# Performance work log

Hardware: AMD Instinct MI355X
Metric: run time of the kernel (lower is better)

The kernel has to match this reference:

```python
import jax, jax.numpy as jnp
import numpy as np

ITERS = 3

def squash(s, axis):
    # v = (|s|^2 / (1 + |s|^2)) * s / |s|
    sn = jnp.sum(s * s, axis=axis, keepdims=True)
    return sn / (1.0 + sn) * s / jnp.sqrt(sn)

def setup_inputs() -> dict:
    key = jax.random.key(0)
    k1, k2 = jax.random.split(key)
    b, B, C, P2, f = 8, 144, 16, 16, 12
    u = jax.random.normal(k1, (b, B, C, P2, f, f), dtype=jnp.float32)
    a = jax.random.uniform(k2, (b, B, f, f), dtype=jnp.float32)
    return {"u": u, "a": a}

def reference(u, a):
    # u: (b, B, C, P2, f, f); a: (b, B, f, f)
    b, B, C, P2, f, _ = u.shape
    # r: (b, B, C, 1, f, f), initialized uniform over C scaled by activation
    r = jnp.broadcast_to(a[:, :, None, None, :, :] * (1.0 / C), (b, B, C, 1, f, f))
    v = None
    for i in range(ITERS):
        c = jax.nn.softmax(r, axis=2)                       # over C
        v = squash(jnp.sum(c * u, axis=1, keepdims=True), axis=3)  # (b,1,C,P2,f,f)
        if i != ITERS - 1:
            r = r + jnp.sum(u * v, axis=3, keepdims=True)   # agreement over psize
    a_out = jnp.sqrt(jnp.sum(v * v, axis=3, keepdims=True))  # (b,1,C,1,f,f)
    return (jnp.squeeze(v, axis=1), jnp.squeeze(a_out, axis=(1, 3)))
```

## Files before the change

kernel.cpp:

```cpp
#include <hip/hip_runtime.h>
#include <math.h>


#define NB 8
#define BDIM 144
#define CDIM 16
#define PDIM 16
#define SDIM 144
#define PT 16
#define BC 16
#define NPT (SDIM / PT)
#define NBC (BDIM / BC)
#define VELEMS (NB * CDIM * PDIM * SDIM)
#define AELEMS (NB * CDIM * SDIM)

__global__ __launch_bounds__(256) void s_kernel(const float* __restrict__ u,
                                                const float* __restrict__ a,
                                                const float* __restrict__ V,
                                                float* __restrict__ s,
                                                int iter) {
  __shared__ float Vt[CDIM][PDIM][PT];
  __shared__ float lbuf[2][CDIM][PT + 1];

  const int tid = threadIdx.x;
  const int pos = tid & 15;
  const int c = tid >> 4;
  const int b = blockIdx.z;
  const int posg = blockIdx.y * PT + pos;
  const int B0 = blockIdx.x * BC;

  if (iter > 0) {
    const int vb = ((b * CDIM + c) * PDIM) * SDIM + posg;
#pragma unroll
    for (int p = 0; p < PDIM; ++p) Vt[c][p][pos] = V[vb + p * SDIM];
  }
  __syncthreads();

  float sacc[PDIM];
#pragma unroll
  for (int p = 0; p < PDIM; ++p) sacc[p] = 0.f;

  for (int Bi = B0; Bi < B0 + BC; ++Bi) {
    float uv[PDIM];
    const float* ub = u + ((size_t)((b * BDIM + Bi) * CDIM + c) * PDIM) * SDIM + posg;
#pragma unroll
    for (int p = 0; p < PDIM; ++p) uv[p] = ub[p * SDIM];

    float w;
    if (iter == 0) {
      w = 1.0f / CDIM;
    } else {
      float dot = 0.f;
#pragma unroll
      for (int p = 0; p < PDIM; ++p) dot += uv[p] * Vt[c][p][pos];
      const float logit = a[(b * BDIM + Bi) * SDIM + posg] * (1.0f / CDIM) + dot;
      const int pb = Bi & 1;
      lbuf[pb][c][pos] = logit;
      __syncthreads();
      float m = -1e30f;
#pragma unroll
      for (int c2 = 0; c2 < CDIM; ++c2) m = fmaxf(m, lbuf[pb][c2][pos]);
      float sum = 0.f;
#pragma unroll
      for (int c2 = 0; c2 < CDIM; ++c2) sum += __expf(lbuf[pb][c2][pos] - m);
      w = __expf(logit - m) / sum;
    }
#pragma unroll
    for (int p = 0; p < PDIM; ++p) sacc[p] += w * uv[p];
  }

  const int sb = ((b * CDIM + c) * PDIM) * SDIM + posg;
#pragma unroll
  for (int p = 0; p < PDIM; ++p) atomicAdd(&s[sb + p * SDIM], sacc[p]);
}

__global__ __launch_bounds__(256) void q_kernel(float* __restrict__ s,
                                                float* __restrict__ V,
                                                float* __restrict__ out_v,
                                                float* __restrict__ out_a,
                                                int iter) {
  const int gid = blockIdx.x * 256 + threadIdx.x;
  const int b = gid / (CDIM * SDIM);
  const int rem = gid - b * (CDIM * SDIM);
  const int c = rem / SDIM;
  const int posg = rem - c * SDIM;
  const int base = ((b * CDIM + c) * PDIM) * SDIM + posg;

  float sv[PDIM];
  float sn = 0.f;
#pragma unroll
  for (int p = 0; p < PDIM; ++p) {
    const float x = s[base + p * SDIM];
    sv[p] = x;
    sn += x * x;
  }
  const float scale = sn / (1.0f + sn) * rsqrtf(sn);

  if (iter < 2) {
#pragma unroll
    for (int p = 0; p < PDIM; ++p) {
      V[base + p * SDIM] += sv[p] * scale;
      s[base + p * SDIM] = 0.f;
    }
  } else {
    float vv = 0.f;
#pragma unroll
    for (int p = 0; p < PDIM; ++p) {
      const float v = sv[p] * scale;
      out_v[base + p * SDIM] = v;
      vv += v * v;
    }
    out_a[gid] = sqrtf(vv);
  }
}

extern "C" void kernel_launch(void* const* d_in, const int* in_sizes, int n_in,
                              void* d_out, int out_size, void* d_ws, size_t ws_size,
                              hipStream_t stream) {
  const float* u = (const float*)d_in[0];
  const float* a = (const float*)d_in[1];
  float* V = (float*)d_ws;
  float* s = V + VELEMS;
  float* out_v = (float*)d_out;
  float* out_a = out_v + VELEMS;

  hipMemsetAsync(d_ws, 0, (size_t)2 * VELEMS * sizeof(float), stream);

  const dim3 gS(NBC, NPT, NB);
  for (int it = 0; it < 3; ++it) {
    s_kernel<<<gS, 256, 0, stream>>>(u, a, V, s, it);
    q_kernel<<<AELEMS / 256, 256, 0, stream>>>(s, V, out_v, out_a, it);
  }
}
```

Before: 356.6 us.

## Prefetch u loads, specialize first iteration, drop softmax max pass, halve B chunk

Restructures the routing kernel. A dedicated path for the first iteration does a plain sum without the softmax. Later iterations double-buffer the u register loads, stage the activation tile in shared memory, and skip the max-subtraction pass in the softmax, using a fast reciprocal. The B chunk per block is halved to raise the number of blocks in flight. This trades more atomics and the loss of the max-stabilized softmax, which could overflow for large logits, for better latency hiding and less per-step work.

```diff
diff --git a/kernel.cpp b/kernel.cpp
--- a/kernel.cpp
+++ b/kernel.cpp
@@ -8,9 +8,10 @@
 #define PDIM 16
 #define SDIM 144
 #define PT 16
-#define BC 16
+#define BC 8
 #define NPT (SDIM / PT)
 #define NBC (BDIM / BC)
+#define USTRIDE (CDIM * PDIM * SDIM)
 #define VELEMS (NB * CDIM * PDIM * SDIM)
 #define AELEMS (NB * CDIM * SDIM)
 
@@ -20,7 +21,8 @@
                                                 float* __restrict__ s,
                                                 int iter) {
   __shared__ float Vt[CDIM][PDIM][PT];
-  __shared__ float lbuf[2][CDIM][PT + 1];
+  __shared__ float ebuf[2][CDIM][PT + 1];
+  __shared__ float atile[BC][PT];
 
   const int tid = threadIdx.x;
   const int pos = tid & 15;
@@ -29,42 +31,62 @@
   const int posg = blockIdx.y * PT + pos;
   const int B0 = blockIdx.x * BC;
 
-  if (iter > 0) {
-    const int vb = ((b * CDIM + c) * PDIM) * SDIM + posg;
-#pragma unroll
-    for (int p = 0; p < PDIM; ++p) Vt[c][p][pos] = V[vb + p * SDIM];
-  }
-  __syncthreads();
+  const float* ubase =
+      u + ((size_t)((b * BDIM + B0) * CDIM + c) * PDIM) * SDIM + posg;
 
   float sacc[PDIM];
 #pragma unroll
   for (int p = 0; p < PDIM; ++p) sacc[p] = 0.f;
 
-  for (int Bi = B0; Bi < B0 + BC; ++Bi) {
-    float uv[PDIM];
-    const float* ub = u + ((size_t)((b * BDIM + Bi) * CDIM + c) * PDIM) * SDIM + posg;
+  if (iter == 0) {
+#pragma unroll 2
+    for (int j = 0; j < BC; ++j) {
+      const float* ub = ubase + (size_t)j * USTRIDE;
 #pragma unroll
-    for (int p = 0; p < PDIM; ++p) uv[p] = ub[p * SDIM];
+      for (int p = 0; p < PDIM; ++p) sacc[p] += ub[p * SDIM];
+    }
+    const int sb = ((b * CDIM + c) * PDIM) * SDIM + posg;
+#pragma unroll
+    for (int p = 0; p < PDIM; ++p)
+      atomicAdd(&s[sb + p * SDIM], sacc[p] * (1.0f / CDIM));
+    return;
+  }
 
-    float w;
-    if (iter == 0) {
-      w = 1.0f / CDIM;
-    } else {
-      float dot = 0.f;
+  {
+    const int vb = ((b * CDIM + c) * PDIM) * SDIM + posg;
 #pragma unroll
-      for (int p = 0; p < PDIM; ++p) dot += uv[p] * Vt[c][p][pos];
-      const float logit = a[(b * BDIM + Bi) * SDIM + posg] * (1.0f / CDIM) + dot;
-      const int pb = Bi & 1;
-      lbuf[pb][c][pos] = logit;
-      __syncthreads();
-      float m = -1e30f;
+    for (int p = 0; p < PDIM; ++p) Vt[c][p][pos] = V[vb + p * SDIM];
+    if (tid < BC * PT) {
+      const int j = tid >> 4;
+      atile[j][pos] =
+          a[(b * BDIM + B0 + j) * SDIM + blockIdx.y * PT + pos] * (1.0f / CDIM);
+    }
+  }
+  __syncthreads();
+
+  float uvbuf[2][PDIM];
 #pragma unroll
-      for (int c2 = 0; c2 < CDIM; ++c2) m = fmaxf(m, lbuf[pb][c2][pos]);
-      float sum = 0.f;
+  for (int p = 0; p < PDIM; ++p) uvbuf[0][p] = ubase[p * SDIM];
+
 #pragma unroll
-      for (int c2 = 0; c2 < CDIM; ++c2) sum += __expf(lbuf[pb][c2][pos] - m);
-      w = __expf(logit - m) / sum;
+  for (int j = 0; j < BC; ++j) {
+    float* uv = uvbuf[j & 1];
+    float* uvn = uvbuf[(j + 1) & 1];
+    if (j + 1 < BC) {
+      const float* ub = ubase + (size_t)(j + 1) * USTRIDE;
+#pragma unroll
+      for (int p = 0; p < PDIM; ++p) uvn[p] = ub[p * SDIM];
     }
+    float dot = 0.f;
+#pragma unroll
+    for (int p = 0; p < PDIM; ++p) dot += uv[p] * Vt[c][p][pos];
+    const float e = __expf(atile[j][pos] + dot);
+    ebuf[j & 1][c][pos] = e;
+    __syncthreads();
+    float sum = 0.f;
+#pragma unroll
+    for (int c2 = 0; c2 < CDIM; ++c2) sum += ebuf[j & 1][c2][pos];
+    const float w = e * __builtin_amdgcn_rcpf(sum);
 #pragma unroll
     for (int p = 0; p < PDIM; ++p) sacc[p] += w * uv[p];
   }
```

Measured after the change: 355.3 us. No clear change (-0.4%).

## Transpose u to position-major layout once, use vectorized loads and shuffle softmax

Applied to the files above, without the earlier changes.

The first pass reads u, writes a transposed copy with psize innermost to workspace, and accumulates the uniform-weight s in the same sweep. Later passes read that copy with float4 loads and do the softmax over C with wave shuffles instead of LDS and barriers. The max subtraction is dropped, and the final activation is taken directly from the squash factor. This adds one full extra write of u (about 100MB) and relies on the logits being small enough that exp does not overflow without the max.

```diff
diff --git a/kernel.cpp b/kernel.cpp
--- a/kernel.cpp
+++ b/kernel.cpp
@@ -7,71 +7,123 @@
 #define CDIM 16
 #define PDIM 16
 #define SDIM 144
-#define PT 16
-#define BC 16
-#define NPT (SDIM / PT)
-#define NBC (BDIM / BC)
-#define VELEMS (NB * CDIM * PDIM * SDIM)
+#define PLANE (PDIM * SDIM)
+#define VELEMS (NB * CDIM * PLANE)
 #define AELEMS (NB * CDIM * SDIM)
+#define UELEMS ((size_t)NB * BDIM * CDIM * PLANE)
+#define LROW 148
 
-__global__ __launch_bounds__(256) void s_kernel(const float* __restrict__ u,
-                                                const float* __restrict__ a,
-                                                const float* __restrict__ V,
-                                                float* __restrict__ s,
-                                                int iter) {
-  __shared__ float Vt[CDIM][PDIM][PT];
-  __shared__ float lbuf[2][CDIM][PT + 1];
+__device__ __forceinline__ float4 ld4(const float* p) { return *(const float4*)p; }
+__device__ __forceinline__ void st4(float* p, float4 v) { *(float4*)p = v; }
 
+__global__ __launch_bounds__(64) void t_kernel(const float* __restrict__ u,
+                                               float* __restrict__ up,
+                                               float* __restrict__ s) {
+  __shared__ float lds[PDIM * LROW];
+  const int l = threadIdx.x;
+  const int b = blockIdx.z, c = blockIdx.y;
+  const int B0 = blockIdx.x * 18;
+
+  float4 sacc[9];
+#pragma unroll
+  for (int k = 0; k < 9; ++k) sacc[k] = make_float4(0.f, 0.f, 0.f, 0.f);
+
+#pragma unroll 1
+  for (int j = 0; j < 18; ++j) {
+    const size_t pbase = (size_t)((b * BDIM + B0 + j) * CDIM + c) * PLANE;
+    float4 ld[9];
+#pragma unroll
+    for (int k = 0; k < 9; ++k) ld[k] = ld4(u + pbase + 4 * (l + 64 * k));
+    __syncthreads();
+#pragma unroll
+    for (int k = 0; k < 9; ++k) {
+      const int flat = 4 * (l + 64 * k);
+      const int p = flat / SDIM;
+      const int pos = flat - p * SDIM;
+      st4(&lds[p * LROW + pos], ld[k]);
+    }
+    __syncthreads();
+#pragma unroll
+    for (int k = 0; k < 9; ++k) {
+      const int flat2 = 4 * (l + 64 * k);
+      const int pos2 = flat2 >> 4;
+      const int p0 = flat2 & 15;
+      float4 o;
+      o.x = lds[(p0 + 0) * LROW + pos2];
+      o.y = lds[(p0 + 1) * LROW + pos2];
+      o.z = lds[(p0 + 2) * LROW + pos2];
+      o.w = lds[(p0 + 3) * LROW + pos2];
+      sacc[k].x += o.x; sacc[k].y += o.y; sacc[k].z += o.z; sacc[k].w += o.w;
+      st4(up + pbase + flat2, o);
+    }
+  }
+  const size_t sbase = (size_t)(b * CDIM + c) * PLANE;
+#pragma unroll
+  for (int k = 0; k < 9; ++k) {
+    const int flat2 = 4 * (l + 64 * k);
+    atomicAdd(&s[sbase + flat2 + 0], sacc[k].x * 0.0625f);
+    atomicAdd(&s[sbase + flat2 + 1], sacc[k].y * 0.0625f);
+    atomicAdd(&s[sbase + flat2 + 2], sacc[k].z * 0.0625f);
+    atomicAdd(&s[sbase + flat2 + 3], sacc[k].w * 0.0625f);
+  }
+}
+
+__global__ __launch_bounds__(256) void s_pass(const float* __restrict__ up,
+                                              const float* __restrict__ a,
+                                              const float* __restrict__ V,
+                                              float* __restrict__ s) {
   const int tid = threadIdx.x;
-  const int pos = tid & 15;
-  const int c = tid >> 4;
+  const int plo = tid & 3;
+  const int c = (tid >> 2) & 15;
+  const int w = tid >> 6;
+  const int posg = blockIdx.y * 16 + (w << 2) + plo;
   const int b = blockIdx.z;
-  const int posg = blockIdx.y * PT + pos;
-  const int B0 = blockIdx.x * BC;
+  const int B0 = blockIdx.x * 16;
 
-  if (iter > 0) {
-    const int vb = ((b * CDIM + c) * PDIM) * SDIM + posg;
+  const size_t ub0 =
+      (size_t)((b * BDIM + B0) * CDIM + c) * PLANE + posg * PDIM;
+  const size_t vb = (size_t)(b * CDIM + c) * PLANE + posg * PDIM;
+
+  float4 Vt[4];
 #pragma unroll
-    for (int p = 0; p < PDIM; ++p) Vt[c][p][pos] = V[vb + p * SDIM];
+  for (int i = 0; i < 4; ++i) Vt[i] = ld4(V + vb + 4 * i);
+
+  float4 sacc[4];
+#pragma unroll
+  for (int i = 0; i < 4; ++i) sacc[i] = make_float4(0.f, 0.f, 0.f, 0.f);
+
+#pragma unroll 2
+  for (int j = 0; j < 16; ++j) {
+    const float* ub = up + ub0 + (size_t)j * (CDIM * PLANE);
+    float4 uv[4];
+#pragma unroll
+    for (int i = 0; i < 4; ++i) uv[i] = ld4(ub + 4 * i);
+
+    float dot = 0.f;
+#pragma unroll
+    for (int i = 0; i < 4; ++i) {
+      dot += uv[i].x * Vt[i].x + uv[i].y * Vt[i].y +
+             uv[i].z * Vt[i].z + uv[i].w * Vt[i].w;
+    }
+    const float av = a[(size_t)(b * BDIM + B0 + j) * SDIM + posg];
+    const float e = __expf(av * 0.0625f + dot);
+    float sum = e;
+#pragma unroll
+    for (int m = 4; m <= 32; m <<= 1) sum += __shfl_xor(sum, m);
+    const float wt = e * __builtin_amdgcn_rcpf(sum);
+#pragma unroll
+    for (int i = 0; i < 4; ++i) {
+      sacc[i].x += wt * uv[i].x; sacc[i].y += wt * uv[i].y;
+      sacc[i].z += wt * uv[i].z; sacc[i].w += wt * uv[i].w;
+    }
   }
-  __syncthreads();
-
-  float sacc[PDIM];
 #pragma unroll
-  for (int p = 0; p < PDIM; ++p) sacc[p] = 0.f;
-
-  for (int Bi = B0; Bi < B0 + BC; ++Bi) {
-    float uv[PDIM];
-    const float* ub = u + ((size_t)((b * BDIM + Bi) * CDIM + c) * PDIM) * SDIM + posg;
-#pragma unroll
-    for (int p = 0; p < PDIM; ++p) uv[p] = ub[p * SDIM];
-
-    float w;
-    if (iter == 0) {
-      w = 1.0f / CDIM;
-    } else {
-      float dot = 0.f;
-#pragma unroll
-      for (int p = 0; p < PDIM; ++p) dot += uv[p] * Vt[c][p][pos];
-      const float logit = a[(b * BDIM + Bi) * SDIM + posg] * (1.0f / CDIM) + dot;
-      const int pb = Bi & 1;
-      lbuf[pb][c][pos] = logit;
-      __syncthreads();
-      float m = -1e30f;
-#pragma unroll
-      for (int c2 = 0; c2 < CDIM; ++c2) m = fmaxf(m, lbuf[pb][c2][pos]);
-      float sum = 0.f;
-#pragma unroll
-      for (int c2 = 0; c2 < CDIM; ++c2) sum += __expf(lbuf[pb][c2][pos] - m);
-      w = __expf(logit - m) / sum;
-    }
-#pragma unroll
-    for (int p = 0; p < PDIM; ++p) sacc[p] += w * uv[p];
+  for (int i = 0; i < 4; ++i) {
+    atomicAdd(&s[vb + 4 * i + 0], sacc[i].x);
+    atomicAdd(&s[vb + 4 * i + 1], sacc[i].y);
+    atomicAdd(&s[vb + 4 * i + 2], sacc[i].z);
+    atomicAdd(&s[vb + 4 * i + 3], sacc[i].w);
   }
-
-  const int sb = ((b * CDIM + c) * PDIM) * SDIM + posg;
-#pragma unroll
-  for (int p = 0; p < PDIM; ++p) atomicAdd(&s[sb + p * SDIM], sacc[p]);
 }
 
 __global__ __launch_bounds__(256) void q_kernel(float* __restrict__ s,
@@ -80,37 +132,46 @@
                                                 float* __restrict__ out_a,
                                                 int iter) {
   const int gid = blockIdx.x * 256 + threadIdx.x;
-  const int b = gid / (CDIM * SDIM);
-  const int rem = gid - b * (CDIM * SDIM);
-  const int c = rem / SDIM;
-  const int posg = rem - c * SDIM;
-  const int base = ((b * CDIM + c) * PDIM) * SDIM + posg;
+  const int posg = gid % SDIM;
+  const int bc = gid / SDIM;
+  const size_t base = (size_t)bc * PLANE + posg * PDIM;
 
-  float sv[PDIM];
+  float4 sv[4];
   float sn = 0.f;
 #pragma unroll
-  for (int p = 0; p < PDIM; ++p) {
-    const float x = s[base + p * SDIM];
-    sv[p] = x;
-    sn += x * x;
+  for (int i = 0; i < 4; ++i) {
+    sv[i] = ld4(s + base + 4 * i);
+    sn += sv[i].x * sv[i].x + sv[i].y * sv[i].y +
+          sv[i].z * sv[i].z + sv[i].w * sv[i].w;
   }
-  const float scale = sn / (1.0f + sn) * rsqrtf(sn);
+  const float g = sn * __builtin_amdgcn_rcpf(1.f + sn);
+  const float sc = g * rsqrtf(sn);
 
   if (iter < 2) {
 #pragma unroll
-    for (int p = 0; p < PDIM; ++p) {
-      V[base + p * SDIM] += sv[p] * scale;
-      s[base + p * SDIM] = 0.f;
+    for (int i = 0; i < 4; ++i) {
+      float4 nv;
+      nv.x = sv[i].x * sc; nv.y = sv[i].y * sc;
+      nv.z = sv[i].z * sc; nv.w = sv[i].w * sc;
+      if (iter == 0) {
+        st4(V + base + 4 * i, nv);
+      } else {
+        float4 ov = ld4(V + base + 4 * i);
+        ov.x += nv.x; ov.y += nv.y; ov.z += nv.z; ov.w += nv.w;
+        st4(V + base + 4 * i, ov);
+      }
+      st4(s + base + 4 * i, make_float4(0.f, 0.f, 0.f, 0.f));
     }
   } else {
-    float vv = 0.f;
+    float* ov = out_v + (size_t)bc * PLANE + posg;
 #pragma unroll
-    for (int p = 0; p < PDIM; ++p) {
-      const float v = sv[p] * scale;
-      out_v[base + p * SDIM] = v;
-      vv += v * v;
+    for (int i = 0; i < 4; ++i) {
+      ov[(4 * i + 0) * SDIM] = sv[i].x * sc;
+      ov[(4 * i + 1) * SDIM] = sv[i].y * sc;
+      ov[(4 * i + 2) * SDIM] = sv[i].z * sc;
+      ov[(4 * i + 3) * SDIM] = sv[i].w * sc;
     }
-    out_a[gid] = sqrtf(vv);
+    out_a[gid] = g;
   }
 }
 
@@ -121,14 +182,16 @@
   const float* a = (const float*)d_in[1];
   float* V = (float*)d_ws;
   float* s = V + VELEMS;
+  float* up = s + VELEMS;
   float* out_v = (float*)d_out;
   float* out_a = out_v + VELEMS;
 
-  hipMemsetAsync(d_ws, 0, (size_t)2 * VELEMS * sizeof(float), stream);
+  hipMemsetAsync(s, 0, (size_t)VELEMS * sizeof(float), stream);
 
-  const dim3 gS(NBC, NPT, NB);
-  for (int it = 0; it < 3; ++it) {
-    s_kernel<<<gS, 256, 0, stream>>>(u, a, V, s, it);
-    q_kernel<<<AELEMS / 256, 256, 0, stream>>>(s, V, out_v, out_a, it);
-  }
+  t_kernel<<<dim3(8, CDIM, NB), 64, 0, stream>>>(u, up, s);
+  q_kernel<<<AELEMS / 256, 256, 0, stream>>>(s, V, out_v, out_a, 0);
+  s_pass<<<dim3(9, 9, NB), 256, 0, stream>>>(up, a, V, s);
+  q_kernel<<<AELEMS / 256, 256, 0, stream>>>(s, V, out_v, out_a, 1);
+  s_pass<<<dim3(9, 9, NB), 256, 0, stream>>>(up, a, V, s);
+  q_kernel<<<AELEMS / 256, 256, 0, stream>>>(s, V, out_v, out_a, 2);
 }
```

Result: slower. 638.7 us (+79.1%).

## Remap s-pass to lane-per-capsule with DPP softmax and atomic-free partial sums

Applied to the files above, without the earlier changes.

Reorganizes the routing s-pass so that each wavefront lane owns one output capsule and four spatial positions. The capsule softmax is now a 16-lane DPP row reduction, replacing the shared-memory buffer and per-iteration __syncthreads. Loads of u, V and a become float4 vectorized, and each block reduces four wavefronts' accumulators through LDS. Partial sums go to 9 per-chunk buffers that q_kernel sums, replacing global atomics and the workspace memset. The cost is a larger register footprint and extra partial-buffer traffic in q_kernel.

```diff
diff --git a/kernel.cpp b/kernel.cpp
--- a/kernel.cpp
+++ b/kernel.cpp
@@ -7,110 +7,147 @@
 #define CDIM 16
 #define PDIM 16
 #define SDIM 144
-#define PT 16
-#define BC 16
-#define NPT (SDIM / PT)
-#define NBC (BDIM / BC)
-#define VELEMS (NB * CDIM * PDIM * SDIM)
+#define PLANE (PDIM * SDIM)
+#define VELEMS (NB * CDIM * PLANE)
 #define AELEMS (NB * CDIM * SDIM)
+#define NCHUNK 9
 
-__global__ __launch_bounds__(256) void s_kernel(const float* __restrict__ u,
-                                                const float* __restrict__ a,
-                                                const float* __restrict__ V,
-                                                float* __restrict__ s,
-                                                int iter) {
-  __shared__ float Vt[CDIM][PDIM][PT];
-  __shared__ float lbuf[2][CDIM][PT + 1];
+__device__ __forceinline__ float4 ld4(const float* p) { return *(const float4*)p; }
+__device__ __forceinline__ void st4(float* p, float4 v) { *(float4*)p = v; }
 
-  const int tid = threadIdx.x;
-  const int pos = tid & 15;
-  const int c = tid >> 4;
+template <int CTRL>
+__device__ __forceinline__ float dpp_mov(float x) {
+  return __int_as_float(__builtin_amdgcn_update_dpp(
+      0, __float_as_int(x), CTRL, 0xF, 0xF, true));
+}
+__device__ __forceinline__ float rowsum16(float x) {
+  x += dpp_mov<0xB1>(x);
+  x += dpp_mov<0x4E>(x);
+  x += dpp_mov<0x124>(x);
+  x += dpp_mov<0x128>(x);
+  return x;
+}
+
+__global__ __launch_bounds__(256, 2) void s_pass(const float* __restrict__ u,
+                                                 const float* __restrict__ a,
+                                                 const float* __restrict__ V,
+                                                 float* __restrict__ spart,
+                                                 int it) {
+  __shared__ float4 red[3 * 64 * 17];
+  const int lane = threadIdx.x & 63;
+  const int w = threadIdx.x >> 6;
+  const int c = lane & 15;
+  const int posq = lane >> 4;
   const int b = blockIdx.z;
-  const int posg = blockIdx.y * PT + pos;
-  const int B0 = blockIdx.x * BC;
+  const int pos0 = blockIdx.y * 16 + posq * 4;
+  const int B0 = blockIdx.x * 16 + w * 4;
 
-  if (iter > 0) {
-    const int vb = ((b * CDIM + c) * PDIM) * SDIM + posg;
+  const float* ub =
+      u + ((size_t)((b * BDIM + B0) * CDIM + c) * PDIM) * SDIM + pos0;
+
+  float4 Vt[16];
+  if (it) {
+    const float* vb = V + ((size_t)(b * CDIM + c) * PDIM) * SDIM + pos0;
 #pragma unroll
-    for (int p = 0; p < PDIM; ++p) Vt[c][p][pos] = V[vb + p * SDIM];
+    for (int p = 0; p < 16; ++p) Vt[p] = ld4(vb + p * SDIM);
+  }
+
+  float4 sacc[16];
+#pragma unroll
+  for (int p = 0; p < 16; ++p) sacc[p] = make_float4(0.f, 0.f, 0.f, 0.f);
+
+#pragma unroll 1
+  for (int j = 0; j < 4; ++j) {
+    const float* uj = ub + (size_t)j * (CDIM * PLANE);
+    float4 uv[16];
+#pragma unroll
+    for (int p = 0; p < 16; ++p) uv[p] = ld4(uj + p * SDIM);
+
+    float4 wt;
+    if (it) {
+      float4 d = make_float4(0.f, 0.f, 0.f, 0.f);
+#pragma unroll
+      for (int p = 0; p < 16; ++p) {
+        d.x += uv[p].x * Vt[p].x; d.y += uv[p].y * Vt[p].y;
+        d.z += uv[p].z * Vt[p].z; d.w += uv[p].w * Vt[p].w;
+      }
+      const float4 a4 = ld4(a + (size_t)(b * BDIM + B0 + j) * SDIM + pos0);
+      float4 e;
+      e.x = __expf(fmaf(a4.x, 0.0625f, d.x));
+      e.y = __expf(fmaf(a4.y, 0.0625f, d.y));
+      e.z = __expf(fmaf(a4.z, 0.0625f, d.z));
+      e.w = __expf(fmaf(a4.w, 0.0625f, d.w));
+      wt.x = e.x * __builtin_amdgcn_rcpf(rowsum16(e.x));
+      wt.y = e.y * __builtin_amdgcn_rcpf(rowsum16(e.y));
+      wt.z = e.z * __builtin_amdgcn_rcpf(rowsum16(e.z));
+      wt.w = e.w * __builtin_amdgcn_rcpf(rowsum16(e.w));
+    } else {
+      wt = make_float4(0.0625f, 0.0625f, 0.0625f, 0.0625f);
+    }
+#pragma unroll
+    for (int p = 0; p < 16; ++p) {
+      sacc[p].x += wt.x * uv[p].x; sacc[p].y += wt.y * uv[p].y;
+      sacc[p].z += wt.z * uv[p].z; sacc[p].w += wt.w * uv[p].w;
+    }
+  }
+
+  if (w > 0) {
+    float4* dst = &red[(w - 1) * 64 * 17 + lane * 17];
+#pragma unroll
+    for (int p = 0; p < 16; ++p) dst[p] = sacc[p];
   }
   __syncthreads();
-
-  float sacc[PDIM];
+  if (w == 0) {
+#pragma unroll 1
+    for (int k = 0; k < 3; ++k) {
+      const float4* src = &red[k * 64 * 17 + lane * 17];
 #pragma unroll
-  for (int p = 0; p < PDIM; ++p) sacc[p] = 0.f;
-
-  for (int Bi = B0; Bi < B0 + BC; ++Bi) {
-    float uv[PDIM];
-    const float* ub = u + ((size_t)((b * BDIM + Bi) * CDIM + c) * PDIM) * SDIM + posg;
+      for (int p = 0; p < 16; ++p) {
+        const float4 x = src[p];
+        sacc[p].x += x.x; sacc[p].y += x.y; sacc[p].z += x.z; sacc[p].w += x.w;
+      }
+    }
+    float* sp = spart + (size_t)blockIdx.x * VELEMS +
+                ((size_t)(b * CDIM + c) * PDIM) * SDIM + pos0;
 #pragma unroll
-    for (int p = 0; p < PDIM; ++p) uv[p] = ub[p * SDIM];
-
-    float w;
-    if (iter == 0) {
-      w = 1.0f / CDIM;
-    } else {
-      float dot = 0.f;
-#pragma unroll
-      for (int p = 0; p < PDIM; ++p) dot += uv[p] * Vt[c][p][pos];
-      const float logit = a[(b * BDIM + Bi) * SDIM + posg] * (1.0f / CDIM) + dot;
-      const int pb = Bi & 1;
-      lbuf[pb][c][pos] = logit;
-      __syncthreads();
-      float m = -1e30f;
-#pragma unroll
-      for (int c2 = 0; c2 < CDIM; ++c2) m = fmaxf(m, lbuf[pb][c2][pos]);
-      float sum = 0.f;
-#pragma unroll
-      for (int c2 = 0; c2 < CDIM; ++c2) sum += __expf(lbuf[pb][c2][pos] - m);
-      w = __expf(logit - m) / sum;
-    }
-#pragma unroll
-    for (int p = 0; p < PDIM; ++p) sacc[p] += w * uv[p];
+    for (int p = 0; p < 16; ++p) st4(sp + p * SDIM, sacc[p]);
   }
-
-  const int sb = ((b * CDIM + c) * PDIM) * SDIM + posg;
-#pragma unroll
-  for (int p = 0; p < PDIM; ++p) atomicAdd(&s[sb + p * SDIM], sacc[p]);
 }
 
-__global__ __launch_bounds__(256) void q_kernel(float* __restrict__ s,
+__global__ __launch_bounds__(256) void q_kernel(const float* __restrict__ spart,
                                                 float* __restrict__ V,
                                                 float* __restrict__ out_v,
                                                 float* __restrict__ out_a,
-                                                int iter) {
+                                                int it) {
   const int gid = blockIdx.x * 256 + threadIdx.x;
-  const int b = gid / (CDIM * SDIM);
-  const int rem = gid - b * (CDIM * SDIM);
-  const int c = rem / SDIM;
-  const int posg = rem - c * SDIM;
-  const int base = ((b * CDIM + c) * PDIM) * SDIM + posg;
+  const int pos = gid % SDIM;
+  const int bc = gid / SDIM;
+  const size_t base = (size_t)bc * PLANE + pos;
 
-  float sv[PDIM];
+  float sv[16];
   float sn = 0.f;
 #pragma unroll
-  for (int p = 0; p < PDIM; ++p) {
-    const float x = s[base + p * SDIM];
+  for (int p = 0; p < 16; ++p) {
+    float x = spart[base + p * SDIM];
+#pragma unroll
+    for (int k = 1; k < NCHUNK; ++k)
+      x += spart[(size_t)k * VELEMS + base + p * SDIM];
     sv[p] = x;
     sn += x * x;
   }
-  const float scale = sn / (1.0f + sn) * rsqrtf(sn);
+  const float g = sn * __builtin_amdgcn_rcpf(1.f + sn);
+  const float sc = g * rsqrtf(sn);
 
-  if (iter < 2) {
+  if (it == 0) {
 #pragma unroll
-    for (int p = 0; p < PDIM; ++p) {
-      V[base + p * SDIM] += sv[p] * scale;
-      s[base + p * SDIM] = 0.f;
-    }
+    for (int p = 0; p < 16; ++p) V[base + p * SDIM] = sv[p] * sc;
+  } else if (it == 1) {
+#pragma unroll
+    for (int p = 0; p < 16; ++p) V[base + p * SDIM] += sv[p] * sc;
   } else {
-    float vv = 0.f;
 #pragma unroll
-    for (int p = 0; p < PDIM; ++p) {
-      const float v = sv[p] * scale;
-      out_v[base + p * SDIM] = v;
-      vv += v * v;
-    }
-    out_a[gid] = sqrtf(vv);
+    for (int p = 0; p < 16; ++p) out_v[base + p * SDIM] = sv[p] * sc;
+    out_a[gid] = g;
   }
 }
 
@@ -120,15 +157,13 @@
   const float* u = (const float*)d_in[0];
   const float* a = (const float*)d_in[1];
   float* V = (float*)d_ws;
-  float* s = V + VELEMS;
+  float* spart = V + VELEMS;
   float* out_v = (float*)d_out;
   float* out_a = out_v + VELEMS;
 
-  hipMemsetAsync(d_ws, 0, (size_t)2 * VELEMS * sizeof(float), stream);
-
-  const dim3 gS(NBC, NPT, NB);
+  const dim3 gS(NCHUNK, 9, NB);
   for (int it = 0; it < 3; ++it) {
-    s_kernel<<<gS, 256, 0, stream>>>(u, a, V, s, it);
-    q_kernel<<<AELEMS / 256, 256, 0, stream>>>(s, V, out_v, out_a, it);
+    s_pass<<<gS, 256, 0, stream>>>(u, a, V, spart, it);
+    q_kernel<<<AELEMS / 256, 256, 0, stream>>>(spart, V, out_v, out_a, it);
   }
 }
```

Result: slower. 382.5 us (+7.3%).
